# Optimization experiments

Hardware: AMD Instinct MI355X
Metric: run time of the kernel (lower is better)

Reference implementation:

```python
import jax, jax.numpy as jnp
import numpy as np

N = 100000   # nodes
E = 1600000  # edges (avg degree 16)
D = 64       # in_dim == emb_dim
L = 3        # num_layers
G = 2000     # graphs in batch
LN_EPS = 1e-5


def setup_inputs() -> dict:
    key = jax.random.key(0)
    ks = jax.random.split(key, 14)
    s = 0.05  # xavier-ish small init scale
    x = jax.random.normal(ks[0], (N, D), jnp.float32)
    edge_index = jax.random.randint(ks[1], (2, E), 0, N, dtype=jnp.int32)
    batch = jnp.sort(jax.random.randint(ks[2], (N,), 0, G, dtype=jnp.int32))
    return {
        "x": x,
        "edge_index": edge_index,
        "batch": batch,
        # stacked per-layer GIN MLP params: Linear(D,D) -> SiLU -> Linear(D,D)
        "W1": jax.random.normal(ks[3], (L, D, D), jnp.float32) * s,
        "b1": jnp.zeros((L, D), jnp.float32),
        "W2": jax.random.normal(ks[4], (L, D, D), jnp.float32) * s,
        "b2": jnp.zeros((L, D), jnp.float32),
        "eps": jnp.zeros((L,), jnp.float32),  # trainable eps, init 0
        "ln_g": jnp.ones((L, D), jnp.float32),
        "ln_b": jnp.zeros((L, D), jnp.float32),
        # gate_nn: Linear(D, D//2) -> SiLU -> Linear(D//2, 1)
        "gw1": jax.random.normal(ks[5], (D, D // 2), jnp.float32) * s,
        "gb1": jnp.zeros((D // 2,), jnp.float32),
        "gw2": jax.random.normal(ks[6], (D // 2, 1), jnp.float32) * s,
        "gb2": jnp.zeros((1,), jnp.float32),
    }


def _layernorm(h, g, b):
    mu = jnp.mean(h, axis=-1, keepdims=True)
    var = jnp.mean(jnp.square(h - mu), axis=-1, keepdims=True)
    return (h - mu) * jax.lax.rsqrt(var + LN_EPS) * g + b


def reference(x, edge_index, batch, W1, b1, W2, b2, eps, ln_g, ln_b, gw1, gb1, gw2, gb2):
    src, dst = edge_index[0], edge_index[1]
    # ---- GIN layers (eval mode: dropout is identity) ----
    for l in range(L):
        agg = jax.ops.segment_sum(x[src], dst, num_segments=N)  # scatter-add of neighbor feats
        h = (1.0 + eps[l]) * x + agg                             # GIN update
        h = jax.nn.silu(h @ W1[l] + b1[l]) @ W2[l] + b2[l]       # 2-layer MLP
        x = _layernorm(h, ln_g[l], ln_b[l])
    # ---- GlobalAttention pooling ----
    gate = (jax.nn.silu(x @ gw1 + gb1) @ gw2 + gb2)[:, 0]        # [N]
    m = jax.ops.segment_max(gate, batch, num_segments=G)         # per-graph max for stability
    e = jnp.exp(gate - m[batch])
    denom = jax.ops.segment_sum(e, batch, num_segments=G)
    a = e / denom[batch]                                         # per-graph softmax
    out = jax.ops.segment_sum(a[:, None] * x, batch, num_segments=G)  # [G, D]
    return out
```

## Files before the change

### kernel.cpp

```cpp
#include <hip/hip_runtime.h>
#include <math.h>

#define NN 100000
#define NE 1600000
#define D 64
#define NG 2000
#define LN_EPS 1e-5f
#define NB ((NN + 255) / 256)
#define NBK NB
#define NTILE ((NN + 63) / 64)
#define EPB 6400
#define NPART (NE / EPB)
#define CAP 6144
#define LSTR 72
#define WFRAG_MLP 24576
#define WFRAG_TOT 26624
#define CONV1K ((NN * D) / 1024)
#define WPREP1K (WFRAG_TOT / 1024)

typedef __attribute__((ext_vector_type(8))) short short8;
typedef __attribute__((ext_vector_type(8))) unsigned short ushort8;
typedef __attribute__((ext_vector_type(4))) float floatx4;

__device__ __forceinline__ unsigned short f2bf(float f) {
    unsigned int u = __float_as_uint(f);
    u += 0x7FFF + ((u >> 16) & 1);
    return (unsigned short)(u >> 16);
}
__device__ __forceinline__ float bfu2f(unsigned short v) {
    return __uint_as_float(((unsigned int)v) << 16);
}

__global__ __launch_bounds__(1024) void k_prep_part(const float* __restrict__ x,
                                                    unsigned short* __restrict__ xb,
                                                    const float* __restrict__ W1,
                                                    const float* __restrict__ W2,
                                                    const float* __restrict__ gw1,
                                                    unsigned short* __restrict__ wfrag,
                                                    const int* __restrict__ src,
                                                    const int* __restrict__ dst,
                                                    int* __restrict__ bcur,
                                                    unsigned int* __restrict__ colbuf) {
    __shared__ int lcnt[NBK];
    __shared__ int lbase[NBK];
    int b = blockIdx.x;
    int tid = threadIdx.x;

    if (b < NPART) {
        int e0 = b * EPB;
        for (int i = tid; i < NBK; i += 1024) lcnt[i] = 0;
        __syncthreads();

        for (int e = tid; e < EPB; e += 1024)
            atomicAdd(&lcnt[dst[e0 + e] >> 8], 1);
        __syncthreads();

        for (int i = tid; i < NBK; i += 1024) {
            int c = lcnt[i];
            lbase[i] = c ? (i * CAP + atomicAdd(&bcur[i * 16], c)) : 0;
            lcnt[i] = 0;
        }
        __syncthreads();

        for (int e = tid; e < EPB; e += 1024) {
            int d = dst[e0 + e];
            int s = src[e0 + e];
            int bk = d >> 8;
            int pos = lbase[bk] + atomicAdd(&lcnt[bk], 1);
            colbuf[pos] = ((unsigned int)s << 8) | (unsigned int)(d & 255);
        }
    } else if (b < NPART + CONV1K) {
        int i = (b - NPART) * 1024 + tid;
        xb[i] = f2bf(x[i]);
    } else {
        int idx = (b - NPART - CONV1K) * 1024 + tid;
        if (idx < WFRAG_MLP) {
            int l = idx / 8192;
            int rem = idx % 8192;
            int mat = rem / 4096;
            int r2 = rem % 4096;
            int ks = r2 / 2048;
            int c = (r2 / 512) % 4;
            int lane = (r2 / 8) % 64;
            int j = r2 % 8;
            int n = lane & 15, q = lane >> 4;
            int k = ks * 32 + q * 8 + j;
            int col = c * 16 + n;
            const float* Wm = mat ? W2 : W1;
            wfrag[idx] = f2bf(Wm[l * 4096 + k * 64 + col]);
        } else {
            int g = idx - WFRAG_MLP;
            int ks = g / 1024;
            int c = (g / 512) % 2;
            int lane = (g / 8) % 64;
            int j = g % 8;
            int n = lane & 15, q = lane >> 4;
            int k = ks * 32 + q * 8 + j;
            wfrag[idx] = f2bf(gw1[k * 32 + c * 16 + n]);
        }
    }
}

__global__ __launch_bounds__(256) void k_bfill(const unsigned int* __restrict__ colbuf,
                                               const int* __restrict__ bcur,
                                               int* __restrict__ rps,
                                               int* __restrict__ rpe,
                                               int* __restrict__ col) {
    __shared__ int lcur[256];
    __shared__ int wsum[4];
    int b = blockIdx.x;
    int ebase = b * CAP;
    int cnt = bcur[b * 16];
    int nb0 = b * 256;
    int nodes = min(256, NN - nb0);
    int tid = threadIdx.x;
    int lane = tid & 63;
    int w = tid >> 6;

    lcur[tid] = 0;
    __syncthreads();

    for (int e = tid; e < cnt; e += 256)
        atomicAdd(&lcur[colbuf[ebase + e] & 255], 1);
    __syncthreads();

    int v = lcur[tid];
    int x = v;
#pragma unroll
    for (int off = 1; off < 64; off <<= 1) {
        int u = __shfl_up(x, off, 64);
        if (lane >= off) x += u;
    }
    if (lane == 63) wsum[w] = x;
    __syncthreads();
    int base = ebase;
    for (int k = 0; k < w; k++) base += wsum[k];
    int rp = base + x - v;
    if (tid < nodes) {
        rps[nb0 + tid] = rp;
        rpe[nb0 + tid] = rp + v;
    }
    lcur[tid] = rp;
    __syncthreads();

    for (int e = tid; e < cnt; e += 256) {
        unsigned int p = colbuf[ebase + e];
        int pos = atomicAdd(&lcur[p & 255], 1);
        col[pos] = p >> 8;
    }
}

template <int LAST>
__global__ __launch_bounds__(512) void k_layer(const unsigned short* __restrict__ xin,
                                               unsigned short* __restrict__ xout,
                                               const int* __restrict__ rps,
                                               const int* __restrict__ rpe,
                                               const int* __restrict__ col,
                                               const float* __restrict__ epsp,
                                               const short8* __restrict__ wf,
                                               const short8* __restrict__ gf,
                                               const float* __restrict__ b1,
                                               const float* __restrict__ b2,
                                               const float* __restrict__ lng,
                                               const float* __restrict__ lnb,
                                               const float* __restrict__ gb1,
                                               const float* __restrict__ gw2,
                                               const float* __restrict__ gb2,
                                               float* __restrict__ gate) {
    __shared__ __align__(16) unsigned short smH[64 * LSTR];
    __shared__ __align__(16) unsigned short smA[4][16 * LSTR];
    int w = threadIdx.x >> 6;
    int lane = threadIdx.x & 63;
    int g = lane >> 3;
    int fl = lane & 7;
    int bl = w * 8 + g;
    int node = blockIdx.x * 64 + bl;
    int nc = min(node, NN - 1);
    int start = rps[nc];
    int end = (node < NN) ? rpe[nc] : start;

    ushort8 xs = *(const ushort8*)(xin + ((size_t)nc << 6) + fl * 8);

    float a0 = 0.f, a1 = 0.f, a2 = 0.f, a3 = 0.f, a4 = 0.f, a5 = 0.f, a6 = 0.f, a7 = 0.f;
    int eb = start;
    for (; eb + 8 <= end; eb += 8) {
        int c = col[eb + fl];
        ushort8 v[8];
#pragma unroll
        for (int j = 0; j < 8; j++) {
            int idx = __shfl(c, g * 8 + j, 64);
            v[j] = *(const ushort8*)(xin + ((size_t)idx << 6) + fl * 8);
        }
#pragma unroll
        for (int j = 0; j < 8; j++) {
            a0 += bfu2f(v[j][0]); a1 += bfu2f(v[j][1]);
            a2 += bfu2f(v[j][2]); a3 += bfu2f(v[j][3]);
            a4 += bfu2f(v[j][4]); a5 += bfu2f(v[j][5]);
            a6 += bfu2f(v[j][6]); a7 += bfu2f(v[j][7]);
        }
    }
    if (eb < end) {
        int cnt = end - eb;
        int c = (fl < cnt) ? col[eb + fl] : 0;
        int j = 0;
        for (; j + 4 <= cnt; j += 4) {
            int i0 = __shfl(c, g * 8 + j, 64);
            int i1 = __shfl(c, g * 8 + j + 1, 64);
            int i2 = __shfl(c, g * 8 + j + 2, 64);
            int i3 = __shfl(c, g * 8 + j + 3, 64);
            ushort8 v0 = *(const ushort8*)(xin + ((size_t)i0 << 6) + fl * 8);
            ushort8 v1 = *(const ushort8*)(xin + ((size_t)i1 << 6) + fl * 8);
            ushort8 v2 = *(const ushort8*)(xin + ((size_t)i2 << 6) + fl * 8);
            ushort8 v3 = *(const ushort8*)(xin + ((size_t)i3 << 6) + fl * 8);
            a0 += bfu2f(v0[0]) + bfu2f(v1[0]) + bfu2f(v2[0]) + bfu2f(v3[0]);
            a1 += bfu2f(v0[1]) + bfu2f(v1[1]) + bfu2f(v2[1]) + bfu2f(v3[1]);
            a2 += bfu2f(v0[2]) + bfu2f(v1[2]) + bfu2f(v2[2]) + bfu2f(v3[2]);
            a3 += bfu2f(v0[3]) + bfu2f(v1[3]) + bfu2f(v2[3]) + bfu2f(v3[3]);
            a4 += bfu2f(v0[4]) + bfu2f(v1[4]) + bfu2f(v2[4]) + bfu2f(v3[4]);
            a5 += bfu2f(v0[5]) + bfu2f(v1[5]) + bfu2f(v2[5]) + bfu2f(v3[5]);
            a6 += bfu2f(v0[6]) + bfu2f(v1[6]) + bfu2f(v2[6]) + bfu2f(v3[6]);
            a7 += bfu2f(v0[7]) + bfu2f(v1[7]) + bfu2f(v2[7]) + bfu2f(v3[7]);
        }
        for (; j < cnt; j++) {
            int i0 = __shfl(c, g * 8 + j, 64);
            ushort8 v0 = *(const ushort8*)(xin + ((size_t)i0 << 6) + fl * 8);
            a0 += bfu2f(v0[0]); a1 += bfu2f(v0[1]);
            a2 += bfu2f(v0[2]); a3 += bfu2f(v0[3]);
            a4 += bfu2f(v0[4]); a5 += bfu2f(v0[5]);
            a6 += bfu2f(v0[6]); a7 += bfu2f(v0[7]);
        }
    }
    {
        float ev = 1.0f + *epsp;
        ushort8 o;
        o[0] = f2bf(ev * bfu2f(xs[0]) + a0);
        o[1] = f2bf(ev * bfu2f(xs[1]) + a1);
        o[2] = f2bf(ev * bfu2f(xs[2]) + a2);
        o[3] = f2bf(ev * bfu2f(xs[3]) + a3);
        o[4] = f2bf(ev * bfu2f(xs[4]) + a4);
        o[5] = f2bf(ev * bfu2f(xs[5]) + a5);
        o[6] = f2bf(ev * bfu2f(xs[6]) + a6);
        o[7] = f2bf(ev * bfu2f(xs[7]) + a7);
        *(ushort8*)(smH + bl * LSTR + fl * 8) = o;
    }
    __syncthreads();

    if (w >= 4) return;
    int n = lane & 15;
    int q = lane >> 4;
    int base = blockIdx.x * 64 + w * 16;

    short8 B1f[2][4], B2f[2][4];
#pragma unroll
    for (int ks = 0; ks < 2; ks++)
#pragma unroll
        for (int c = 0; c < 4; c++) {
            B1f[ks][c] = wf[(ks * 4 + c) * 64 + lane];
            B2f[ks][c] = wf[512 + (ks * 4 + c) * 64 + lane];
        }
    short8 B3f[2][2];
    if (LAST) {
#pragma unroll
        for (int ks = 0; ks < 2; ks++)
#pragma unroll
            for (int c = 0; c < 2; c++)
                B3f[ks][c] = gf[(ks * 2 + c) * 64 + lane];
    }

    float b1v[4], b2v[4], lgv[4], lbv[4];
#pragma unroll
    for (int c = 0; c < 4; c++) {
        b1v[c] = b1[c * 16 + n];
        b2v[c] = b2[c * 16 + n];
        lgv[c] = lng[c * 16 + n];
        lbv[c] = lnb[c * 16 + n];
    }
    float gb1v[2], gw2v[2], gb2v = 0.f;
    if (LAST) {
        gb1v[0] = gb1[n]; gb1v[1] = gb1[16 + n];
        gw2v[0] = gw2[n]; gw2v[1] = gw2[16 + n];
        gb2v = gb2[0];
    }

    unsigned short* aw = smA[w];

    const short8* hp = (const short8*)(smH + (w * 16 + n) * LSTR);
    short8 A0 = hp[q];
    short8 A1 = hp[4 + q];

    floatx4 acc1[4];
#pragma unroll
    for (int c = 0; c < 4; c++) {
        floatx4 a = {b1v[c], b1v[c], b1v[c], b1v[c]};
        a = __builtin_amdgcn_mfma_f32_16x16x32_bf16(A0, B1f[0][c], a, 0, 0, 0);
        a = __builtin_amdgcn_mfma_f32_16x16x32_bf16(A1, B1f[1][c], a, 0, 0, 0);
        acc1[c] = a;
    }

#pragma unroll
    for (int c = 0; c < 4; c++)
#pragma unroll
        for (int r = 0; r < 4; r++) {
            float v = acc1[c][r];
            v = v / (1.0f + __expf(-v));
            aw[(q * 4 + r) * LSTR + c * 16 + n] = f2bf(v);
        }

    const short8* ap = (const short8*)(aw + n * LSTR);
    short8 A20 = ap[q];
    short8 A21 = ap[4 + q];

    floatx4 acc2[4];
#pragma unroll
    for (int c = 0; c < 4; c++) {
        floatx4 a = {b2v[c], b2v[c], b2v[c], b2v[c]};
        a = __builtin_amdgcn_mfma_f32_16x16x32_bf16(A20, B2f[0][c], a, 0, 0, 0);
        a = __builtin_amdgcn_mfma_f32_16x16x32_bf16(A21, B2f[1][c], a, 0, 0, 0);
        acc2[c] = a;
    }

    float mu[4], inv[4];
#pragma unroll
    for (int r = 0; r < 4; r++) {
        float s = acc2[0][r] + acc2[1][r] + acc2[2][r] + acc2[3][r];
#pragma unroll
        for (int off = 1; off < 16; off <<= 1) s += __shfl_xor(s, off, 64);
        mu[r] = s * (1.0f / 64.0f);
        float d0 = acc2[0][r] - mu[r], d1 = acc2[1][r] - mu[r];
        float d2 = acc2[2][r] - mu[r], d3 = acc2[3][r] - mu[r];
        float vv = d0 * d0 + d1 * d1 + d2 * d2 + d3 * d3;
#pragma unroll
        for (int off = 1; off < 16; off <<= 1) vv += __shfl_xor(vv, off, 64);
        inv[r] = rsqrtf(vv * (1.0f / 64.0f) + LN_EPS);
    }

#pragma unroll
    for (int c = 0; c < 4; c++)
#pragma unroll
        for (int r = 0; r < 4; r++) {
            int onode = base + q * 4 + r;
            float o = (acc2[c][r] - mu[r]) * inv[r] * lgv[c] + lbv[c];
            unsigned short ob = f2bf(o);
            if (onode < NN) xout[((size_t)onode << 6) + c * 16 + n] = ob;
            if (LAST) aw[(q * 4 + r) * LSTR + c * 16 + n] = ob;
        }

    if (LAST) {
        short8 G0 = ap[q];
        short8 G1 = ap[4 + q];
        floatx4 acc3[2];
#pragma unroll
        for (int c = 0; c < 2; c++) {
            floatx4 a = {gb1v[c], gb1v[c], gb1v[c], gb1v[c]};
            a = __builtin_amdgcn_mfma_f32_16x16x32_bf16(G0, B3f[0][c], a, 0, 0, 0);
            a = __builtin_amdgcn_mfma_f32_16x16x32_bf16(G1, B3f[1][c], a, 0, 0, 0);
            acc3[c] = a;
        }
#pragma unroll
        for (int r = 0; r < 4; r++) {
            float v0 = acc3[0][r];
            v0 = v0 / (1.0f + __expf(-v0));
            float v1 = acc3[1][r];
            v1 = v1 / (1.0f + __expf(-v1));
            float gsum = v0 * gw2v[0] + v1 * gw2v[1];
#pragma unroll
            for (int off = 1; off < 16; off <<= 1) gsum += __shfl_xor(gsum, off, 64);
            int onode = base + q * 4 + r;
            if (n == 0 && onode < NN) gate[onode] = gsum + gb2v;
        }
    }
}

__global__ __launch_bounds__(256) void k_pool(const unsigned short* __restrict__ xf,
                                              const float* __restrict__ gate,
                                              const int* __restrict__ batch,
                                              float* __restrict__ out) {
    __shared__ float redm[4];
    __shared__ float reds[4];
    __shared__ float racc[4][D];
    int g = blockIdx.x;
    int w = threadIdx.x >> 6;
    int lane = threadIdx.x & 63;

    int lo = 0, hi = NN;
    while (lo < hi) { int mid = (lo + hi) >> 1; if (batch[mid] < g) lo = mid + 1; else hi = mid; }
    int start = lo;
    hi = NN;
    while (lo < hi) { int mid = (lo + hi) >> 1; if (batch[mid] < g + 1) lo = mid + 1; else hi = mid; }
    int end = lo;

    if (start >= end) {
        if (w == 0) out[((size_t)g << 6) + lane] = 0.0f;
        return;
    }

    float m = -INFINITY;
    for (int i = start + (int)threadIdx.x; i < end; i += 256) m = fmaxf(m, gate[i]);
#pragma unroll
    for (int mm = 32; mm >= 1; mm >>= 1) m = fmaxf(m, __shfl_xor(m, mm, 64));
    if (lane == 0) redm[w] = m;
    __syncthreads();
    m = fmaxf(fmaxf(redm[0], redm[1]), fmaxf(redm[2], redm[3]));

    float s = 0.0f;
    for (int i = start + (int)threadIdx.x; i < end; i += 256) s += __expf(gate[i] - m);
#pragma unroll
    for (int mm = 32; mm >= 1; mm >>= 1) s += __shfl_xor(s, mm, 64);
    if (lane == 0) reds[w] = s;
    __syncthreads();
    s = (reds[0] + reds[1]) + (reds[2] + reds[3]);

    float acc = 0.0f;
    for (int i = start + w; i < end; i += 4)
        acc += __expf(gate[i] - m) * bfu2f(xf[((size_t)i << 6) + lane]);
    racc[w][lane] = acc;
    __syncthreads();
    if (w == 0)
        out[((size_t)g << 6) + lane] =
            ((racc[0][lane] + racc[1][lane]) + (racc[2][lane] + racc[3][lane])) / s;
}

extern "C" void kernel_launch(void* const* d_in, const int* in_sizes, int n_in,
                              void* d_out, int out_size, void* d_ws, size_t ws_size,
                              hipStream_t stream) {
    const float* x   = (const float*)d_in[0];
    const int* ei    = (const int*)d_in[1];
    const int* batch = (const int*)d_in[2];
    const float* W1  = (const float*)d_in[3];
    const float* b1  = (const float*)d_in[4];
    const float* W2  = (const float*)d_in[5];
    const float* b2  = (const float*)d_in[6];
    const float* eps = (const float*)d_in[7];
    const float* lng = (const float*)d_in[8];
    const float* lnb = (const float*)d_in[9];
    const float* gw1 = (const float*)d_in[10];
    const float* gb1 = (const float*)d_in[11];
    const float* gw2 = (const float*)d_in[12];
    const float* gb2 = (const float*)d_in[13];

    const int* src = ei;
    const int* dst = ei + NE;

    unsigned short* xb    = (unsigned short*)d_ws;
    unsigned short* h     = xb + (size_t)NN * D;
    float* gate           = (float*)(h + (size_t)NN * D);
    int* rps              = (int*)(gate + NN);
    int* rpe              = rps + NN;
    int* colbuf           = rpe + NN;
    int* col              = colbuf + (size_t)NBK * CAP;
    int* bcur             = col + (size_t)NBK * CAP;
    unsigned short* wfrag = (unsigned short*)(bcur + NBK * 16);

    float* out = (float*)d_out;

    hipMemsetAsync(bcur, 0, NBK * 16 * sizeof(int), stream);
    k_prep_part<<<NPART + CONV1K + WPREP1K, 1024, 0, stream>>>(
        x, xb, W1, W2, gw1, wfrag, src, dst, bcur, (unsigned int*)colbuf);
    k_bfill<<<NBK, 256, 0, stream>>>((unsigned int*)colbuf, bcur, rps, rpe, col);

    const short8* wf0 = (const short8*)(wfrag);
    const short8* wf1 = (const short8*)(wfrag + 8192);
    const short8* wf2 = (const short8*)(wfrag + 16384);
    const short8* gf  = (const short8*)(wfrag + WFRAG_MLP);

    k_layer<0><<<NTILE, 512, 0, stream>>>(xb, h, rps, rpe, col, eps + 0, wf0, gf,
        b1 + 0 * D, b2 + 0 * D, lng + 0 * D, lnb + 0 * D, gb1, gw2, gb2, gate);

    k_layer<0><<<NTILE, 512, 0, stream>>>(h, xb, rps, rpe, col, eps + 1, wf1, gf,
        b1 + 1 * D, b2 + 1 * D, lng + 1 * D, lnb + 1 * D, gb1, gw2, gb2, gate);

    k_layer<1><<<NTILE, 512, 0, stream>>>(xb, h, rps, rpe, col, eps + 2, wf2, gf,
        b1 + 2 * D, b2 + 2 * D, lng + 2 * D, lnb + 2 * D, gb1, gw2, gb2, gate);

    k_pool<<<NG, 256, 0, stream>>>(h, gate, batch, out);
}
```

Before: 286.6 us.

## Gather neighbours per-wave in MFMA layout, drop block barrier, halve block size

The neighbour aggregation is reorganised so each 64-lane wave handles its own 16 nodes directly in the MFMA row layout: each node gets 4 lanes of 16 features, and the wave walks windows of 4 edges per node. Each wave now writes only its own LDS slice, so the block-wide __syncthreads and the idle half of the 512-thread block go away, and the kernel launches with 256 threads. The cost is load imbalance: every wave loops to the maximum degree among its 16 nodes, with predicated lanes, and there are half as many waves gathering per block.

```diff
diff --git a/kernel.cpp b/kernel.cpp
--- a/kernel.cpp
+++ b/kernel.cpp
@@ -151,7 +151,7 @@
 }
 
 template <int LAST>
-__global__ __launch_bounds__(512) void k_layer(const unsigned short* __restrict__ xin,
+__global__ __launch_bounds__(256) void k_layer(const unsigned short* __restrict__ xin,
                                                unsigned short* __restrict__ xout,
                                                const int* __restrict__ rps,
                                                const int* __restrict__ rpe,
@@ -167,88 +167,71 @@
                                                const float* __restrict__ gw2,
                                                const float* __restrict__ gb2,
                                                float* __restrict__ gate) {
-    __shared__ __align__(16) unsigned short smH[64 * LSTR];
+    __shared__ __align__(16) unsigned short smH[4][16 * LSTR];
     __shared__ __align__(16) unsigned short smA[4][16 * LSTR];
     int w = threadIdx.x >> 6;
     int lane = threadIdx.x & 63;
-    int g = lane >> 3;
-    int fl = lane & 7;
-    int bl = w * 8 + g;
-    int node = blockIdx.x * 64 + bl;
+    int n = lane & 15;
+    int fl = lane >> 4;
+    int base = blockIdx.x * 64 + w * 16;
+    int node = base + n;
     int nc = min(node, NN - 1);
-    int start = rps[nc];
-    int end = (node < NN) ? rpe[nc] : start;
-
-    ushort8 xs = *(const ushort8*)(xin + ((size_t)nc << 6) + fl * 8);
-
-    float a0 = 0.f, a1 = 0.f, a2 = 0.f, a3 = 0.f, a4 = 0.f, a5 = 0.f, a6 = 0.f, a7 = 0.f;
-    int eb = start;
-    for (; eb + 8 <= end; eb += 8) {
-        int c = col[eb + fl];
-        ushort8 v[8];
-#pragma unroll
-        for (int j = 0; j < 8; j++) {
-            int idx = __shfl(c, g * 8 + j, 64);
-            v[j] = *(const ushort8*)(xin + ((size_t)idx << 6) + fl * 8);
-        }
-#pragma unroll
-        for (int j = 0; j < 8; j++) {
-            a0 += bfu2f(v[j][0]); a1 += bfu2f(v[j][1]);
-            a2 += bfu2f(v[j][2]); a3 += bfu2f(v[j][3]);
-            a4 += bfu2f(v[j][4]); a5 += bfu2f(v[j][5]);
-            a6 += bfu2f(v[j][6]); a7 += bfu2f(v[j][7]);
-        }
-    }
-    if (eb < end) {
-        int cnt = end - eb;
-        int c = (fl < cnt) ? col[eb + fl] : 0;
-        int j = 0;
-        for (; j + 4 <= cnt; j += 4) {
-            int i0 = __shfl(c, g * 8 + j, 64);
-            int i1 = __shfl(c, g * 8 + j + 1, 64);
-            int i2 = __shfl(c, g * 8 + j + 2, 64);
-            int i3 = __shfl(c, g * 8 + j + 3, 64);
-            ushort8 v0 = *(const ushort8*)(xin + ((size_t)i0 << 6) + fl * 8);
-            ushort8 v1 = *(const ushort8*)(xin + ((size_t)i1 << 6) + fl * 8);
-            ushort8 v2 = *(const ushort8*)(xin + ((size_t)i2 << 6) + fl * 8);
-            ushort8 v3 = *(const ushort8*)(xin + ((size_t)i3 << 6) + fl * 8);
-            a0 += bfu2f(v0[0]) + bfu2f(v1[0]) + bfu2f(v2[0]) + bfu2f(v3[0]);
-            a1 += bfu2f(v0[1]) + bfu2f(v1[1]) + bfu2f(v2[1]) + bfu2f(v3[1]);
-            a2 += bfu2f(v0[2]) + bfu2f(v1[2]) + bfu2f(v2[2]) + bfu2f(v3[2]);
-            a3 += bfu2f(v0[3]) + bfu2f(v1[3]) + bfu2f(v2[3]) + bfu2f(v3[3]);
-            a4 += bfu2f(v0[4]) + bfu2f(v1[4]) + bfu2f(v2[4]) + bfu2f(v3[4]);
-            a5 += bfu2f(v0[5]) + bfu2f(v1[5]) + bfu2f(v2[5]) + bfu2f(v3[5]);
-            a6 += bfu2f(v0[6]) + bfu2f(v1[6]) + bfu2f(v2[6]) + bfu2f(v3[6]);
-            a7 += bfu2f(v0[7]) + bfu2f(v1[7]) + bfu2f(v2[7]) + bfu2f(v3[7]);
-        }
-        for (; j < cnt; j++) {
-            int i0 = __shfl(c, g * 8 + j, 64);
-            ushort8 v0 = *(const ushort8*)(xin + ((size_t)i0 << 6) + fl * 8);
-            a0 += bfu2f(v0[0]); a1 += bfu2f(v0[1]);
-            a2 += bfu2f(v0[2]); a3 += bfu2f(v0[3]);
-            a4 += bfu2f(v0[4]); a5 += bfu2f(v0[5]);
-            a6 += bfu2f(v0[6]); a7 += bfu2f(v0[7]);
-        }
-    }
+    int st = rps[nc];
+    int en = (node < NN) ? rpe[nc] : st;
+    float ev = 1.0f + *epsp;
+
+    float a[16];
+#pragma unroll
+    for (int e = 0; e < 16; e++) a[e] = 0.f;
+
+    int nwin = (en - st + 3) >> 2;
+#pragma unroll
+    for (int off = 1; off < 64; off <<= 1) nwin = max(nwin, __shfl_xor(nwin, off, 64));
+
+    const unsigned short* xrow = xin + ((size_t)nc << 6) + fl * 16;
+    ushort8 xs0 = *(const ushort8*)(xrow);
+    ushort8 xs1 = *(const ushort8*)(xrow + 8);
+
+    for (int t = 0; t < nwin; t++) {
+        int b0 = st + t * 4;
+        int ce = b0 + fl;
+        int c0 = (ce < en) ? col[ce] : -1;
+        ushort8 v0[4], v1[4];
+        unsigned int m = 0;
+#pragma unroll
+        for (int j = 0; j < 4; j++) {
+            int idx = __shfl(c0, n + j * 16, 64);
+            if (idx >= 0) {
+                const ushort8* p = (const ushort8*)(xin + ((size_t)idx << 6) + fl * 16);
+                v0[j] = p[0];
+                v1[j] = p[1];
+                m |= 1u << j;
+            }
+        }
+#pragma unroll
+        for (int j = 0; j < 4; j++)
+            if (m & (1u << j)) {
+#pragma unroll
+                for (int e = 0; e < 8; e++) {
+                    a[e] += bfu2f(v0[j][e]);
+                    a[8 + e] += bfu2f(v1[j][e]);
+                }
+            }
+    }
+
     {
-        float ev = 1.0f + *epsp;
-        ushort8 o;
-        o[0] = f2bf(ev * bfu2f(xs[0]) + a0);
-        o[1] = f2bf(ev * bfu2f(xs[1]) + a1);
-        o[2] = f2bf(ev * bfu2f(xs[2]) + a2);
-        o[3] = f2bf(ev * bfu2f(xs[3]) + a3);
-        o[4] = f2bf(ev * bfu2f(xs[4]) + a4);
-        o[5] = f2bf(ev * bfu2f(xs[5]) + a5);
-        o[6] = f2bf(ev * bfu2f(xs[6]) + a6);
-        o[7] = f2bf(ev * bfu2f(xs[7]) + a7);
-        *(ushort8*)(smH + bl * LSTR + fl * 8) = o;
-    }
-    __syncthreads();
-
-    if (w >= 4) return;
-    int n = lane & 15;
-    int q = lane >> 4;
-    int base = blockIdx.x * 64 + w * 16;
+        ushort8 o0, o1;
+#pragma unroll
+        for (int e = 0; e < 8; e++) {
+            o0[e] = f2bf(ev * bfu2f(xs0[e]) + a[e]);
+            o1[e] = f2bf(ev * bfu2f(xs1[e]) + a[8 + e]);
+        }
+        unsigned short* hw = smH[w] + n * LSTR + fl * 16;
+        *(ushort8*)(hw) = o0;
+        *(ushort8*)(hw + 8) = o1;
+    }
+
+    int q = fl;
 
     short8 B1f[2][4], B2f[2][4];
 #pragma unroll
@@ -284,17 +267,17 @@
 
     unsigned short* aw = smA[w];
 
-    const short8* hp = (const short8*)(smH + (w * 16 + n) * LSTR);
+    const short8* hp = (const short8*)(smH[w] + n * LSTR);
     short8 A0 = hp[q];
     short8 A1 = hp[4 + q];
 
     floatx4 acc1[4];
 #pragma unroll
     for (int c = 0; c < 4; c++) {
-        floatx4 a = {b1v[c], b1v[c], b1v[c], b1v[c]};
-        a = __builtin_amdgcn_mfma_f32_16x16x32_bf16(A0, B1f[0][c], a, 0, 0, 0);
-        a = __builtin_amdgcn_mfma_f32_16x16x32_bf16(A1, B1f[1][c], a, 0, 0, 0);
-        acc1[c] = a;
+        floatx4 a1 = {b1v[c], b1v[c], b1v[c], b1v[c]};
+        a1 = __builtin_amdgcn_mfma_f32_16x16x32_bf16(A0, B1f[0][c], a1, 0, 0, 0);
+        a1 = __builtin_amdgcn_mfma_f32_16x16x32_bf16(A1, B1f[1][c], a1, 0, 0, 0);
+        acc1[c] = a1;
     }
 
 #pragma unroll
@@ -313,10 +296,10 @@
     floatx4 acc2[4];
 #pragma unroll
     for (int c = 0; c < 4; c++) {
-        floatx4 a = {b2v[c], b2v[c], b2v[c], b2v[c]};
-        a = __builtin_amdgcn_mfma_f32_16x16x32_bf16(A20, B2f[0][c], a, 0, 0, 0);
-        a = __builtin_amdgcn_mfma_f32_16x16x32_bf16(A21, B2f[1][c], a, 0, 0, 0);
-        acc2[c] = a;
+        floatx4 a2 = {b2v[c], b2v[c], b2v[c], b2v[c]};
+        a2 = __builtin_amdgcn_mfma_f32_16x16x32_bf16(A20, B2f[0][c], a2, 0, 0, 0);
+        a2 = __builtin_amdgcn_mfma_f32_16x16x32_bf16(A21, B2f[1][c], a2, 0, 0, 0);
+        acc2[c] = a2;
     }
 
     float mu[4], inv[4];
@@ -351,10 +334,10 @@
         floatx4 acc3[2];
 #pragma unroll
         for (int c = 0; c < 2; c++) {
-            floatx4 a = {gb1v[c], gb1v[c], gb1v[c], gb1v[c]};
-            a = __builtin_amdgcn_mfma_f32_16x16x32_bf16(G0, B3f[0][c], a, 0, 0, 0);
-            a = __builtin_amdgcn_mfma_f32_16x16x32_bf16(G1, B3f[1][c], a, 0, 0, 0);
-            acc3[c] = a;
+            floatx4 a3 = {gb1v[c], gb1v[c], gb1v[c], gb1v[c]};
+            a3 = __builtin_amdgcn_mfma_f32_16x16x32_bf16(G0, B3f[0][c], a3, 0, 0, 0);
+            a3 = __builtin_amdgcn_mfma_f32_16x16x32_bf16(G1, B3f[1][c], a3, 0, 0, 0);
+            acc3[c] = a3;
         }
 #pragma unroll
         for (int r = 0; r < 4; r++) {
@@ -463,13 +446,13 @@
     const short8* wf2 = (const short8*)(wfrag + 16384);
     const short8* gf  = (const short8*)(wfrag + WFRAG_MLP);
 
-    k_layer<0><<<NTILE, 512, 0, stream>>>(xb, h, rps, rpe, col, eps + 0, wf0, gf,
+    k_layer<0><<<NTILE, 256, 0, stream>>>(xb, h, rps, rpe, col, eps + 0, wf0, gf,
         b1 + 0 * D, b2 + 0 * D, lng + 0 * D, lnb + 0 * D, gb1, gw2, gb2, gate);
 
-    k_layer<0><<<NTILE, 512, 0, stream>>>(h, xb, rps, rpe, col, eps + 1, wf1, gf,
+    k_layer<0><<<NTILE, 256, 0, stream>>>(h, xb, rps, rpe, col, eps + 1, wf1, gf,
         b1 + 1 * D, b2 + 1 * D, lng + 1 * D, lnb + 1 * D, gb1, gw2, gb2, gate);
 
-    k_layer<1><<<NTILE, 512, 0, stream>>>(xb, h, rps, rpe, col, eps + 2, wf2, gf,
+    k_layer<1><<<NTILE, 256, 0, stream>>>(xb, h, rps, rpe, col, eps + 2, wf2, gf,
         b1 + 2 * D, b2 + 2 * D, lng + 2 * D, lnb + 2 * D, gb1, gw2, gb2, gate);
 
     k_pool<<<NG, 256, 0, stream>>>(h, gate, batch, out);
```

Result: no change. 283.3 us (-1.1%).
